# Kernel tuning notes

Measured on AMD Instinct MI355X. Metric: run time of the kernel, lower is better.

The kernel has to match this reference:

```python
import jax, jax.numpy as jnp
import numpy as np

N, E, G = 40000, 640000, 64
D_IN, D_EMB, D_HID, D_OUT = 128, 128, 128, 36


def setup_inputs() -> dict:
    key = jax.random.key(0)
    ks = jax.random.split(key, 12)
    x = jax.random.normal(ks[0], (N, D_IN), dtype=jnp.float32)
    edge_weight = jax.random.uniform(ks[1], (E,), dtype=jnp.float32)
    rho = jax.random.uniform(ks[2], (G,), dtype=jnp.float32)
    edge_index = jax.random.randint(ks[3], (2, E), 0, N, dtype=jnp.int32)
    batch = jnp.sort(jax.random.randint(ks[4], (N,), 0, G, dtype=jnp.int32))
    def lin(k, fi, fo):
        s = 1.0 / np.sqrt(fi)
        return jax.random.normal(k, (fi, fo), dtype=jnp.float32) * s
    conv_w = lin(ks[5], D_IN, D_EMB)
    conv_b = jnp.zeros((D_EMB,), jnp.float32)
    w1 = lin(ks[6], 2 * D_EMB + 1, D_HID); b1 = jnp.zeros((D_HID,), jnp.float32)
    w2 = lin(ks[7], D_HID, D_HID);        b2 = jnp.zeros((D_HID,), jnp.float32)
    w3 = lin(ks[8], D_HID, D_OUT);        b3 = jnp.zeros((D_OUT,), jnp.float32)
    return dict(x=x, edge_weight=edge_weight, rho=rho, conv_w=conv_w, conv_b=conv_b,
                w1=w1, b1=b1, w2=w2, b2=b2, w3=w3, b3=b3,
                edge_index=edge_index, batch=batch)


def _gcn_conv(h, edge_index, ew, W, b):
    # PyG GCNConv: add self-loops (weight 1), symmetric deg^-1/2 normalization,
    # linear transform, gather-scale-scatter aggregation, bias.
    n = h.shape[0]
    loop = jnp.arange(n, dtype=edge_index.dtype)
    src = jnp.concatenate([edge_index[0], loop])
    dst = jnp.concatenate([edge_index[1], loop])
    w_all = jnp.concatenate([ew, jnp.ones((n,), ew.dtype)])
    deg = jax.ops.segment_sum(w_all, dst, num_segments=n)
    dinv = jnp.where(deg > 0, jax.lax.rsqrt(deg), 0.0)
    norm = dinv[src] * w_all * dinv[dst]          # [E+N]
    hW = h @ W                                    # [N, D_EMB]
    msg = hW[src] * norm[:, None]                 # [E+N, D_EMB]
    return jax.ops.segment_sum(msg, dst, num_segments=n) + b


def reference(x, edge_weight, rho, conv_w, conv_b, w1, b1, w2, b2, w3, b3,
              edge_index, batch):
    h = jax.nn.relu(_gcn_conv(x, edge_index, edge_weight, conv_w, conv_b))
    g = G
    cnt = jax.ops.segment_sum(jnp.ones((h.shape[0],), h.dtype), batch, num_segments=g)
    hmax = jax.ops.segment_max(h, batch, num_segments=g)
    hmax = jnp.where(cnt[:, None] > 0, hmax, 0.0)
    hsum = jax.ops.segment_sum(h, batch, num_segments=g)
    hmean = hsum / jnp.maximum(cnt, 1.0)[:, None]
    hg = jnp.concatenate([hmax, hmean, rho[:, None]], axis=1)  # [G, 2*D_EMB+1]
    z = jax.nn.relu(hg @ w1 + b1)
    z = jax.nn.relu(z @ w2 + b2)
    return z @ w3 + b3
```

## Files before the change

kernel.cpp:

```cpp
#include <hip/hip_runtime.h>
#include <hip/hip_bf16.h>
#include <hip/hip_fp16.h>

static __device__ __forceinline__ float relu_f(float v) { return v > 0.f ? v : 0.f; }

typedef _Float16 half8 __attribute__((ext_vector_type(8)));
typedef float floatx4 __attribute__((ext_vector_type(4)));


__global__ void cast_init_kernel(const float4* __restrict__ x4, __half2* __restrict__ xh2,
                                 int n4, int* __restrict__ indeg, int n,
                                 float* __restrict__ gmax, float* __restrict__ gsum,
                                 float* __restrict__ gcnt, int gch, int g,
                                 const float* __restrict__ W, _Float16* __restrict__ wt) {
  int i = blockIdx.x * blockDim.x + threadIdx.x;
  if (i < n4) {
    float4 v = x4[i];
    xh2[2 * i + 0] = __floats2half2_rn(v.x, v.y);
    xh2[2 * i + 1] = __floats2half2_rn(v.z, v.w);
  }
  if (i < n) indeg[i] = 0;
  if (i < gch) { gmax[i] = 0.f; gsum[i] = 0.f; }
  if (i < g) gcnt[i] = 0.f;
  if (i < 128 * 128) {
    int k = i >> 7, nn = i & 127;
    wt[nn * 128 + k] = (_Float16)W[i];
  }
}

__global__ void count_rank_kernel(const int* __restrict__ dst, int* __restrict__ indeg,
                                  int* __restrict__ rank, int E) {
  int e = blockIdx.x * blockDim.x + threadIdx.x;
  if (e >= E) return;
  rank[e] = atomicAdd(&indeg[dst[e]], 1);
}


__global__ __launch_bounds__(1024) void scan_reduce_kernel(const int* __restrict__ indeg,
                                                           int* __restrict__ bsum, int n) {
  int i = blockIdx.x * 1024 + threadIdx.x;
  int v = (i < n) ? ((indeg[i] + 7) & ~7) : 0;
  #pragma unroll
  for (int off = 32; off; off >>= 1) v += __shfl_down(v, off, 64);
  __shared__ int ws[16];
  int lane = threadIdx.x & 63, wid = threadIdx.x >> 6;
  if (lane == 0) ws[wid] = v;
  __syncthreads();
  if (threadIdx.x == 0) {
    int s = 0;
    #pragma unroll
    for (int j = 0; j < 16; ++j) s += ws[j];
    bsum[blockIdx.x] = s;
  }
}

__global__ __launch_bounds__(1024) void scan_write_kernel(const int* __restrict__ indeg,
    const int* __restrict__ bsum, int* __restrict__ rowptr, int n, int nb) {
  int i = blockIdx.x * 1024 + threadIdx.x;
  int v = (i < n) ? ((indeg[i] + 7) & ~7) : 0;
  int lane = threadIdx.x & 63, wid = threadIdx.x >> 6;
  int inc = v;
  #pragma unroll
  for (int off = 1; off < 64; off <<= 1) {
    int u = __shfl_up(inc, off, 64);
    if (lane >= off) inc += u;
  }
  __shared__ int wtot[16];
  __shared__ int s_off;
  if (lane == 63) wtot[wid] = inc;
  if (threadIdx.x < 64) {
    int acc = 0;
    for (int base = 0; base < nb; base += 64) {
      int idx = base + (int)threadIdx.x;
      int val = (idx < nb && idx < (int)blockIdx.x) ? bsum[idx] : 0;
      #pragma unroll
      for (int off = 32; off; off >>= 1) val += __shfl_down(val, off, 64);
      if (threadIdx.x == 0) acc += val;
    }
    if (threadIdx.x == 0) s_off = acc;
  }
  __syncthreads();
  int woff = 0;
  for (int j = 0; j < wid; ++j) woff += wtot[j];
  int excl = s_off + woff + inc - v;
  if (i < n) {
    rowptr[i + 1] = excl + v;
    if (i == 0) rowptr[0] = 0;
  }
}

__global__ void edge_fill_kernel(const int* __restrict__ src, const int* __restrict__ dst,
                                 const float* __restrict__ ew, const int* __restrict__ rank,
                                 const int* __restrict__ rowptr, int2* __restrict__ epack,
                                 int E) {
  int e = blockIdx.x * blockDim.x + threadIdx.x;
  if (e >= E) return;
  int d = dst[e];
  int slot = rowptr[d] + rank[e];
  epack[slot] = make_int2(src[e], __float_as_int(ew[e]));
}

__global__ void row_dinv_kernel(const int* __restrict__ rowptr, const int* __restrict__ indeg,
                                int2* __restrict__ epack, float* __restrict__ dinv, int n) {
  int i = blockIdx.x * blockDim.x + threadIdx.x;
  if (i >= n) return;
  int s = rowptr[i];
  int re = s + indeg[i];
  int e = rowptr[i + 1];
  float d = 1.0f;
  for (int j = s; j < re; ++j) d += __int_as_float(epack[j].y);
  for (int j = re; j < e; ++j) epack[j] = make_int2(0, 0);
  dinv[i] = (d > 0.f) ? rsqrtf(d) : 0.f;
}


__global__ __launch_bounds__(256) void aggregate_kernel(const half8* __restrict__ xh8,
    const float* __restrict__ dinv, const int* __restrict__ rowptr,
    const int2* __restrict__ epack, half8* __restrict__ aggh8, int n) {
  int gid = blockIdx.x * blockDim.x + threadIdx.x;
  int lane = gid & 63;
  int grp = lane >> 4, sub = lane & 15;
  int node = (gid >> 6) * 4 + grp;
  if (node >= n) return;
  float dn = dinv[node];
  half8 xv = xh8[(size_t)node * 16 + sub];
  float sw = dn * dn;
  float acc[8];
  #pragma unroll
  for (int c = 0; c < 8; ++c) acc[c] = sw * (float)xv[c];
  int s = rowptr[node], e = rowptr[node + 1];
  for (int j = s; j < e; j += 8) {
    int2 pk[8];
    #pragma unroll
    for (int u = 0; u < 8; ++u) pk[u] = epack[j + u];
    half8 hx[8];
    float dw[8];
    #pragma unroll
    for (int u = 0; u < 8; ++u) {
      hx[u] = xh8[(size_t)pk[u].x * 16 + sub];
      dw[u] = dinv[pk[u].x];
    }
    #pragma unroll
    for (int u = 0; u < 8; ++u) {
      float w = dw[u] * __int_as_float(pk[u].y) * dn;
      #pragma unroll
      for (int c = 0; c < 8; ++c) acc[c] += w * (float)hx[u][c];
    }
  }
  half8 outv;
  #pragma unroll
  for (int c = 0; c < 8; ++c) outv[c] = (_Float16)acc[c];
  aggh8[(size_t)node * 16 + sub] = outv;
}


__global__ __launch_bounds__(256) void gemm_pool_kernel(const _Float16* __restrict__ aggh,
    const _Float16* __restrict__ wt, const float* __restrict__ bias,
    const int* __restrict__ batch, float* __restrict__ gmax, float* __restrict__ gsum,
    float* __restrict__ gcnt, int n) {
  __shared__ float sH[64 * 129];
  __shared__ int sBatch[64];
  int tid = threadIdx.x;
  int w = tid >> 6, lane = tid & 63;
  int quad = lane >> 4, c15 = lane & 15;
  int row0 = blockIdx.x * 64;
  int nb = n - row0; if (nb > 64) nb = 64;

  float bb[8];
  #pragma unroll
  for (int j = 0; j < 8; ++j) bb[j] = bias[j * 16 + c15];

  int arow = row0 + w * 16 + c15;
  if (arow >= n) arow = n - 1;
  const half8* aptr = (const half8*)(aggh + (size_t)arow * 128 + quad * 8);

  floatx4 acc[8] = {};
  #pragma unroll
  for (int ks = 0; ks < 4; ++ks) {
    half8 af = aptr[ks * 4];
    #pragma unroll
    for (int j = 0; j < 8; ++j) {
      const half8* bptr =
          (const half8*)(wt + (size_t)(j * 16 + c15) * 128 + ks * 32 + quad * 8);
      acc[j] = __builtin_amdgcn_mfma_f32_16x16x32_f16(af, *bptr, acc[j], 0, 0, 0);
    }
  }

  if (tid < nb) sBatch[tid] = batch[row0 + tid];

  #pragma unroll
  for (int j = 0; j < 8; ++j) {
    int col = j * 16 + c15;
    #pragma unroll
    for (int r = 0; r < 4; ++r) {
      int row = w * 16 + quad * 4 + r;
      if (row < nb) sH[row * 129 + col] = relu_f(acc[j][r] + bb[j]);
    }
  }
  __syncthreads();

  if (tid < 128) {
    int c = tid;
    int cur = sBatch[0];
    float mx = 0.f, sm = 0.f;
    int cnt = 0;
    for (int r = 0; r < nb; ++r) {
      int g = sBatch[r];
      if (g != cur) {
        atomicMax((int*)&gmax[cur * 128 + c], __float_as_int(mx));
        atomicAdd(&gsum[cur * 128 + c], sm);
        if (c == 0) atomicAdd(&gcnt[cur], (float)cnt);
        mx = 0.f; sm = 0.f; cnt = 0; cur = g;
      }
      float v = sH[r * 129 + c];
      mx = fmaxf(mx, v);
      sm += v;
      ++cnt;
    }
    atomicMax((int*)&gmax[cur * 128 + c], __float_as_int(mx));
    atomicAdd(&gsum[cur * 128 + c], sm);
    if (c == 0) atomicAdd(&gcnt[cur], (float)cnt);
  }
}


__global__ __launch_bounds__(128) void mlp_kernel(const float* __restrict__ gmax,
    const float* __restrict__ gsum, const float* __restrict__ gcnt,
    const float* __restrict__ rho,
    const float* __restrict__ w1, const float* __restrict__ b1,
    const float* __restrict__ w2, const float* __restrict__ b2,
    const float* __restrict__ w3, const float* __restrict__ b3,
    float* __restrict__ out) {
  __shared__ float s_in[257];
  __shared__ float s_z1[128];
  __shared__ float s_z2[128];
  int g = blockIdx.x, t = threadIdx.x;
  float inv_cnt = 1.f / fmaxf(gcnt[g], 1.f);
  s_in[t] = gmax[g * 128 + t];
  s_in[128 + t] = gsum[g * 128 + t] * inv_cnt;
  if (t == 0) s_in[256] = rho[g];
  __syncthreads();
  float s = b1[t];
  for (int k = 0; k < 257; ++k) s += s_in[k] * w1[k * 128 + t];
  s_z1[t] = relu_f(s);
  __syncthreads();
  s = b2[t];
  for (int k = 0; k < 128; ++k) s += s_z1[k] * w2[k * 128 + t];
  s_z2[t] = relu_f(s);
  __syncthreads();
  if (t < 36) {
    s = b3[t];
    for (int k = 0; k < 128; ++k) s += s_z2[k] * w3[k * 36 + t];
    out[g * 36 + t] = s;
  }
}


extern "C" void kernel_launch(void* const* d_in, const int* in_sizes, int n_in,
                              void* d_out, int out_size, void* d_ws, size_t ws_size,
                              hipStream_t stream) {
  const float* x      = (const float*)d_in[0];
  const float* ew     = (const float*)d_in[1];
  const float* rho    = (const float*)d_in[2];
  const float* conv_w = (const float*)d_in[3];
  const float* conv_b = (const float*)d_in[4];
  const float* w1 = (const float*)d_in[5];
  const float* b1 = (const float*)d_in[6];
  const float* w2 = (const float*)d_in[7];
  const float* b2 = (const float*)d_in[8];
  const float* w3 = (const float*)d_in[9];
  const float* b3 = (const float*)d_in[10];
  const int* eidx  = (const int*)d_in[11];
  const int* batch = (const int*)d_in[12];

  const int N = in_sizes[0] / 128;
  const int E = in_sizes[1];
  const int G = in_sizes[2];
  const int* srcp = eidx;
  const int* dstp = eidx + E;

  const int NB = (N + 1023) / 1024;
  const int EPAD = E + 8 * N;

  char* p = (char*)d_ws;
  auto carve = [&](size_t bytes) { char* r = p; p += (bytes + 255) & ~(size_t)255; return (void*)r; };
  float*    dinv   = (float*)   carve((size_t)N * 4);
  int*      indeg  = (int*)     carve((size_t)N * 4);
  int*      rowptr = (int*)     carve((size_t)(N + 1) * 4);
  int*      rank   = (int*)     carve((size_t)E * 4);
  int*      bsum   = (int*)     carve((size_t)NB * 4);
  int2*     epack  = (int2*)    carve((size_t)EPAD * 8);
  __half2*  xh     = (__half2*) carve((size_t)N * 128 * 2);
  _Float16* aggh   = (_Float16*)carve((size_t)N * 128 * 2);
  _Float16* wt     = (_Float16*)carve((size_t)128 * 128 * 2);
  float*    gmax   = (float*)   carve((size_t)G * 128 * 4);
  float*    gsum   = (float*)   carve((size_t)G * 128 * 4);
  float*    gcnt   = (float*)   carve((size_t)G * 4);

  const int n4 = N * 32;

  cast_init_kernel<<<(n4 + 255) / 256, 256, 0, stream>>>((const float4*)x, xh, n4,
                                                         indeg, N, gmax, gsum, gcnt,
                                                         G * 128, G, conv_w, wt);
  count_rank_kernel<<<(E + 255) / 256, 256, 0, stream>>>(dstp, indeg, rank, E);
  scan_reduce_kernel<<<NB, 1024, 0, stream>>>(indeg, bsum, N);
  scan_write_kernel<<<NB, 1024, 0, stream>>>(indeg, bsum, rowptr, N, NB);
  edge_fill_kernel<<<(E + 255) / 256, 256, 0, stream>>>(srcp, dstp, ew, rank, rowptr, epack, E);
  row_dinv_kernel<<<(N + 255) / 256, 256, 0, stream>>>(rowptr, indeg, epack, dinv, N);
  aggregate_kernel<<<(N + 15) / 16, 256, 0, stream>>>((const half8*)xh, dinv, rowptr, epack,
                                                      (half8*)aggh, N);
  gemm_pool_kernel<<<(N + 63) / 64, 256, 0, stream>>>(aggh, wt, conv_b, batch,
                                                      gmax, gsum, gcnt, N);
  mlp_kernel<<<G, 128, 0, stream>>>(gmax, gsum, gcnt, rho, w1, b1, w2, b2, w3, b3,
                                    (float*)d_out);
}
```

Baseline: 209.7 us.

## Fuse neighbor aggregation into the GEMM+pooling kernel via shared memory

```diff
diff --git a/kernel.cpp b/kernel.cpp
--- a/kernel.cpp
+++ b/kernel.cpp
@@ -114,79 +114,79 @@
 }
 
 
-__global__ __launch_bounds__(256) void aggregate_kernel(const half8* __restrict__ xh8,
+__global__ __launch_bounds__(256) void agg_gemm_pool_kernel(const half8* __restrict__ xh8,
     const float* __restrict__ dinv, const int* __restrict__ rowptr,
-    const int2* __restrict__ epack, half8* __restrict__ aggh8, int n) {
-  int gid = blockIdx.x * blockDim.x + threadIdx.x;
-  int lane = gid & 63;
-  int grp = lane >> 4, sub = lane & 15;
-  int node = (gid >> 6) * 4 + grp;
-  if (node >= n) return;
-  float dn = dinv[node];
-  half8 xv = xh8[(size_t)node * 16 + sub];
-  float sw = dn * dn;
-  float acc[8];
-  #pragma unroll
-  for (int c = 0; c < 8; ++c) acc[c] = sw * (float)xv[c];
-  int s = rowptr[node], e = rowptr[node + 1];
-  for (int j = s; j < e; j += 8) {
-    int2 pk[8];
-    #pragma unroll
-    for (int u = 0; u < 8; ++u) pk[u] = epack[j + u];
-    half8 hx[8];
-    float dw[8];
-    #pragma unroll
-    for (int u = 0; u < 8; ++u) {
-      hx[u] = xh8[(size_t)pk[u].x * 16 + sub];
-      dw[u] = dinv[pk[u].x];
-    }
-    #pragma unroll
-    for (int u = 0; u < 8; ++u) {
-      float w = dw[u] * __int_as_float(pk[u].y) * dn;
-      #pragma unroll
-      for (int c = 0; c < 8; ++c) acc[c] += w * (float)hx[u][c];
-    }
-  }
-  half8 outv;
-  #pragma unroll
-  for (int c = 0; c < 8; ++c) outv[c] = (_Float16)acc[c];
-  aggh8[(size_t)node * 16 + sub] = outv;
-}
-
-
-__global__ __launch_bounds__(256) void gemm_pool_kernel(const _Float16* __restrict__ aggh,
-    const _Float16* __restrict__ wt, const float* __restrict__ bias,
-    const int* __restrict__ batch, float* __restrict__ gmax, float* __restrict__ gsum,
-    float* __restrict__ gcnt, int n) {
+    const int2* __restrict__ epack, const _Float16* __restrict__ wt,
+    const float* __restrict__ bias, const int* __restrict__ batch,
+    float* __restrict__ gmax, float* __restrict__ gsum, float* __restrict__ gcnt, int n) {
   __shared__ float sH[64 * 129];
+  _Float16* sAgg = (_Float16*)sH;
   __shared__ int sBatch[64];
   int tid = threadIdx.x;
   int w = tid >> 6, lane = tid & 63;
+  int grp = lane >> 4, sub = lane & 15;
   int quad = lane >> 4, c15 = lane & 15;
   int row0 = blockIdx.x * 64;
   int nb = n - row0; if (nb > 64) nb = 64;
 
+  #pragma unroll
+  for (int it = 0; it < 4; ++it) {
+    int rloc = w * 16 + it * 4 + grp;
+    int node = row0 + rloc;
+    if (node >= n) node = n - 1;
+    float dn = dinv[node];
+    half8 xv = xh8[(size_t)node * 16 + sub];
+    float sw = dn * dn;
+    float acc[8];
+    #pragma unroll
+    for (int c = 0; c < 8; ++c) acc[c] = sw * (float)xv[c];
+    int s = rowptr[node], e = rowptr[node + 1];
+    for (int j = s; j < e; j += 8) {
+      int2 pk[8];
+      #pragma unroll
+      for (int u = 0; u < 8; ++u) pk[u] = epack[j + u];
+      half8 hx[8];
+      float dw[8];
+      #pragma unroll
+      for (int u = 0; u < 8; ++u) {
+        hx[u] = xh8[(size_t)pk[u].x * 16 + sub];
+        dw[u] = dinv[pk[u].x];
+      }
+      #pragma unroll
+      for (int u = 0; u < 8; ++u) {
+        float wgt = dw[u] * __int_as_float(pk[u].y) * dn;
+        #pragma unroll
+        for (int c = 0; c < 8; ++c) acc[c] += wgt * (float)hx[u][c];
+      }
+    }
+    half8 outv;
+    #pragma unroll
+    for (int c = 0; c < 8; ++c) outv[c] = (_Float16)acc[c];
+    *(half8*)&sAgg[rloc * 136 + sub * 8] = outv;
+  }
+  __syncthreads();
+
+  half8 af[4];
+  #pragma unroll
+  for (int ks = 0; ks < 4; ++ks)
+    af[ks] = *(const half8*)&sAgg[(w * 16 + c15) * 136 + ks * 32 + quad * 8];
+  if (tid < nb) sBatch[tid] = batch[row0 + tid];
+  __syncthreads();
+
   float bb[8];
   #pragma unroll
   for (int j = 0; j < 8; ++j) bb[j] = bias[j * 16 + c15];
 
-  int arow = row0 + w * 16 + c15;
-  if (arow >= n) arow = n - 1;
-  const half8* aptr = (const half8*)(aggh + (size_t)arow * 128 + quad * 8);
-
   floatx4 acc[8] = {};
   #pragma unroll
   for (int ks = 0; ks < 4; ++ks) {
-    half8 af = aptr[ks * 4];
     #pragma unroll
     for (int j = 0; j < 8; ++j) {
       const half8* bptr =
           (const half8*)(wt + (size_t)(j * 16 + c15) * 128 + ks * 32 + quad * 8);
-      acc[j] = __builtin_amdgcn_mfma_f32_16x16x32_f16(af, *bptr, acc[j], 0, 0, 0);
-    }
-  }
-
-  if (tid < nb) sBatch[tid] = batch[row0 + tid];
+      acc[j] = __builtin_amdgcn_mfma_f32_16x16x32_f16(af[ks], *bptr, acc[j], 0, 0, 0);
+    }
+  }
 
   #pragma unroll
   for (int j = 0; j < 8; ++j) {
@@ -291,7 +291,6 @@
   int*      bsum   = (int*)     carve((size_t)NB * 4);
   int2*     epack  = (int2*)    carve((size_t)EPAD * 8);
   __half2*  xh     = (__half2*) carve((size_t)N * 128 * 2);
-  _Float16* aggh   = (_Float16*)carve((size_t)N * 128 * 2);
   _Float16* wt     = (_Float16*)carve((size_t)128 * 128 * 2);
   float*    gmax   = (float*)   carve((size_t)G * 128 * 4);
   float*    gsum   = (float*)   carve((size_t)G * 128 * 4);
@@ -307,10 +306,9 @@
   scan_write_kernel<<<NB, 1024, 0, stream>>>(indeg, bsum, rowptr, N, NB);
   edge_fill_kernel<<<(E + 255) / 256, 256, 0, stream>>>(srcp, dstp, ew, rank, rowptr, epack, E);
   row_dinv_kernel<<<(N + 255) / 256, 256, 0, stream>>>(rowptr, indeg, epack, dinv, N);
-  aggregate_kernel<<<(N + 15) / 16, 256, 0, stream>>>((const half8*)xh, dinv, rowptr, epack,
-                                                      (half8*)aggh, N);
-  gemm_pool_kernel<<<(N + 63) / 64, 256, 0, stream>>>(aggh, wt, conv_b, batch,
-                                                      gmax, gsum, gcnt, N);
+  agg_gemm_pool_kernel<<<(N + 63) / 64, 256, 0, stream>>>((const half8*)xh, dinv, rowptr,
+                                                          epack, wt, conv_b, batch,
+                                                          gmax, gsum, gcnt, N);
   mlp_kernel<<<G, 128, 0, stream>>>(gmax, gsum, gcnt, rho, w1, b1, w2, b2, w3, b3,
                                     (float*)d_out);
 }
```

Measured after the change: 206.0 us. No clear change (-1.8%).
